# Optimization experiments

Measured on AMD Instinct MI355X. Metric: run time of the kernel, lower is better.

Reference implementation:

```python
import jax, jax.numpy as jnp
import numpy as np
from jax import lax

N_IN, N_H = 3, 2
N_REC = N_IN + N_H  # 5 qubits in the recurrent cell


def _ry(theta):
    # theta: (B,) -> (B, 2, 2) complex64 RY matrices
    c = jnp.cos(theta * 0.5).astype(jnp.complex64)
    s = jnp.sin(theta * 0.5).astype(jnp.complex64)
    return jnp.stack([jnp.stack([c, -s], -1), jnp.stack([s, c], -1)], -2)


def _rot(phi, theta, omega):
    # PennyLane Rot(phi, theta, omega) = RZ(omega) @ RY(theta) @ RZ(phi)
    c = jnp.cos(theta * 0.5)
    s = jnp.sin(theta * 0.5)
    ep = jnp.exp(-0.5j * (phi + omega))  # e^{-i(phi+omega)/2}
    em = jnp.exp(0.5j * (phi - omega))   # e^{+i(phi-omega)/2}
    m = jnp.stack([jnp.stack([ep * c, -em * s], -1),
                   jnp.stack([jnp.conj(em) * s, jnp.conj(ep) * c], -1)], -2)
    return m.astype(jnp.complex64)


def _apply1q(state, U, wire, n):
    # state: (B, 2**n); wire 0 is most significant (PennyLane convention)
    L, R = 2 ** wire, 2 ** (n - wire - 1)
    st = state.reshape(-1, L, 2, R)
    sub = 'bij,bljr->blir' if U.ndim == 3 else 'ij,bljr->blir'
    return jnp.einsum(sub, U, st).reshape(state.shape)


def _cnot_perm(c, t, n):
    # CNOT is a fixed basis permutation: flip target bit where control bit set
    cbit, tbit = 1 << (n - 1 - c), 1 << (n - 1 - t)
    idx = np.arange(2 ** n)
    return np.where(idx & cbit, idx ^ tbit, idx)


def _entangle(state, weights, n):
    # StronglyEntanglingLayers: per-wire Rot, then CNOT ring with range r
    n_layers = weights.shape[0]
    for l in range(n_layers):
        for w in range(n):
            state = _apply1q(state, _rot(weights[l, w, 0], weights[l, w, 1], weights[l, w, 2]), w, n)
        r = (l % (n - 1)) + 1
        for w in range(n):
            state = state[:, _cnot_perm(w, (w + r) % n, n)]
    return state


def _expz(state, wire, n):
    # <Z_wire> = P(0) - P(1)
    L, R = 2 ** wire, 2 ** (n - wire - 1)
    p = (state.real ** 2 + state.imag ** 2).reshape(-1, L, 2, R).sum((1, 3))
    return p[:, 0] - p[:, 1]


def _init_state(batch, n):
    s = jnp.zeros((batch, 2 ** n), jnp.complex64)
    return s.at[:, 0].set(1.0)


def _cell(x, h, w_rec):
    # batched qrnn_cell: RY-encode x on wires 0..2, h on wires 3..4, entangle, read Z(3),Z(4)
    state = _init_state(x.shape[0], N_REC)
    for i in range(N_IN):
        state = _apply1q(state, _ry(x[:, i]), i, N_REC)
    for j in range(N_H):
        state = _apply1q(state, _ry(h[:, j]), N_IN + j, N_REC)
    state = _entangle(state, w_rec, N_REC)
    return jnp.stack([_expz(state, N_IN + j, N_REC) for j in range(N_H)], -1)


def _readout(h, w_out):
    # batched qnn_readout: 2-qubit circuit, Z(0) expval
    state = _init_state(h.shape[0], N_H)
    for j in range(N_H):
        state = _apply1q(state, _ry(h[:, j]), j, N_H)
    state = _entangle(state, w_out, N_H)
    return _expz(state, 0, N_H)[:, None]


def setup_inputs() -> dict:
    key = jax.random.key(0)
    k1, k2, k3 = jax.random.split(key, 3)
    T, B = 32, 8192
    x_seq = jax.random.normal(k1, (T, B, N_IN), jnp.float32)
    w_rec = jax.random.normal(k2, (2, N_REC, 3), jnp.float32)
    w_out = jax.random.normal(k3, (2, N_H, 3), jnp.float32)
    return {"x_seq": x_seq, "w_rec": w_rec, "w_out": w_out}


def reference(x_seq, w_rec, w_out):
    B = x_seq.shape[1]

    def step(h, xt):
        return _cell(xt, h, w_rec), None

    h, _ = lax.scan(step, jnp.zeros((B, N_H), jnp.float32), x_seq)
    return _readout(h, w_out)  # (B, 1)
```

## Files before the change

### kernel.cpp

```cpp
#include <hip/hip_runtime.h>
#include <math.h>


constexpr int cnot_ct(int idx, int c, int t) {
    return (idx & (1 << (4 - c))) ? (idx ^ (1 << (4 - t))) : idx;
}
constexpr int Pfwd_ct(int x, int r) {
    for (int w = 4; w >= 0; --w) x = cnot_ct(x, w, (w + r) % 5);
    return x;
}
constexpr int Pinv_ct(int x, int r) {
    for (int w = 0; w <= 4; ++w) x = cnot_ct(x, w, (w + r) % 5);
    return x;
}
static_assert(Pinv_ct(Pfwd_ct(13, 1), 1) == 13, "inv1");
static_assert(Pinv_ct(Pfwd_ct(22, 2), 2) == 22, "inv2");

constexpr int GMASK[10] = {16, 8, 4, 2, 1,
                           Pfwd_ct(16,1), Pfwd_ct(8,1), Pfwd_ct(4,1), Pfwd_ct(2,1), Pfwd_ct(1,1)};
constexpr int fmask_l1(int pb) {
    int f = 0;
    for (int b = 0; b < 5; ++b) if ((Pinv_ct(1 << b, 1) >> pb) & 1) f |= 1 << b;
    return f;
}
constexpr int FMASK[10] = {16, 8, 4, 2, 1,
                           fmask_l1(4), fmask_l1(3), fmask_l1(2), fmask_l1(1), fmask_l1(0)};
constexpr int cinv_ct(int x) { return Pinv_ct(Pinv_ct(x, 1), 2); }
constexpr int fmask_fin(int pb) {
    int f = 0;
    for (int b = 0; b < 5; ++b) if ((cinv_ct(1 << b) >> pb) & 1) f |= 1 << b;
    return f;
}
constexpr int SF3 = fmask_fin(1);
constexpr int SF4 = fmask_fin(0);

constexpr bool gates_straddle() {
    for (int g = 0; g < 10; ++g)
        if (!(__builtin_popcount(GMASK[g] & FMASK[g]) & 1)) return false;
    return true;
}
static_assert(gates_straddle(), "GMASK/FMASK straddle");

constexpr unsigned span3_ct(int a, int b, int c) {
    unsigned m = 0;
    for (int i = 0; i < 8; ++i) {
        int v = ((i & 1) ? a : 0) ^ ((i & 2) ? b : 0) ^ ((i & 4) ? c : 0);
        m |= 1u << v;
    }
    return m;
}
static_assert(span3_ct(1, 2, 7) == 0xFFu, "butterfly {1,2,7} spans lanes 0..7");

__device__ __forceinline__ int pinv_rt(int x, int r) {
    #pragma unroll
    for (int w = 0; w < 5; ++w) {
        int cbit = 1 << (4 - w), tbit = 1 << (4 - ((w + r) % 5));
        if (x & cbit) x ^= tbit;
    }
    return x;
}

__device__ __forceinline__ float Wsel(int r, int d) {
    float b, c;
    if (d == 0)      { b =  2.f / 3.f; c = 0.f; }
    else if (d == 1) { b = -1.f / 3.f; c =  0.57735026918962576f; }
    else             { b = -1.f / 3.f; c = -0.57735026918962576f; }
    return (r == 0) ? (1.f / 3.f) : ((r == 1) ? b : c);
}

template<int CTRL> __device__ __forceinline__ float dppf(float x) {
    return __int_as_float(__builtin_amdgcn_mov_dpp(__float_as_int(x), CTRL, 0xF, 0xF, true));
}
template<int PL> __device__ __forceinline__ float mvf(float x) {
    if constexpr (PL == 1)      return dppf<0xB1>(x);
    else if constexpr (PL == 2) return dppf<0x4E>(x);
    else if constexpr (PL == 7) return dppf<0x141>(x);
    else if constexpr (PL == 8) return dppf<0x128>(x);
    else { static_assert(PL == 1 || PL == 2 || PL == 7 || PL == 8, "mask"); return x; }
}

template<int g>
__device__ __forceinline__ void gate_full(float (&ar)[32], float (&ai)[32],
                                          float c, float s) {
    constexpr int m = GMASK[g], F = FMASK[g];
    #pragma unroll
    for (int i = 0; i < 32; ++i) {
        if ((__builtin_popcount(i & F) & 1) == 0) {
            const int j = i ^ m;
            const float r0 = ar[i], i0 = ai[i], r1 = ar[j], i1 = ai[j];
            ar[i] = c * r0 - s * r1;  ai[i] = c * i0 - s * i1;
            ar[j] = s * r0 + c * r1;  ai[j] = s * i0 + c * i1;
        }
    }
}

__global__ __launch_bounds__(256, 2) void qrnn_fused(
    const float* __restrict__ x_seq, const float* __restrict__ w_rec,
    const float* __restrict__ w_out, float* __restrict__ out, int B) {

    __shared__ __align__(16) float4 xs4[16 * 33];
    __shared__ __align__(16) float A2s[18 * 28];
    __shared__ float CgS[10], SgS[10];
    __shared__ float P0c[32], P0s[32], E1c[32], E1s[32];
    __shared__ float RC[16];
    __shared__ __align__(16) float Cm_pool[16 * 19 * 33];
    float* const Qs  = Cm_pool;
    float* const P1s = Cm_pool + 512;

    const int tloc = threadIdx.x;
    const int grp  = tloc >> 4;
    const int k    = tloc & 15;
    const int b0   = blockIdx.x * 16;
    const int b    = b0 + grp;

    #pragma unroll
    for (int qq = 0; qq < 2; ++qq) {
        const int p = tloc + qq * 256;
        const int ts = p >> 4, lbs = p & 15;
        const int gidx = (ts * B + (b0 + lbs)) * 3;
        float4 v;
        v.x = x_seq[gidx]; v.y = x_seq[gidx + 1]; v.z = x_seq[gidx + 2]; v.w = 0.f;
        xs4[lbs * 33 + ts] = v;
    }

    if (tloc < 10) {
        const float th = w_rec[(tloc / 5) * 15 + (tloc % 5) * 3 + 1];
        CgS[tloc] = cosf(0.5f * th);
        SgS[tloc] = sinf(0.5f * th);
    } else if (tloc >= 32 && tloc < 96) {
        const int idx = tloc - 32;
        const int i = idx & 31;
        float ang = 0.f;
        if (idx < 32) {
            #pragma unroll
            for (int w = 0; w < 5; ++w)
                ang += (((i >> (4 - w)) & 1) ? 0.5f : -0.5f) * w_rec[w * 3 + 0];
            P0c[i] = cosf(ang); P0s[i] = sinf(ang);
        } else {
            const int j = pinv_rt(i, 1);
            #pragma unroll
            for (int w = 0; w < 5; ++w) {
                ang += (((i >> (4 - w)) & 1) ? 0.5f : -0.5f) * w_rec[w * 3 + 2];
                ang += (((j >> (4 - w)) & 1) ? 0.5f : -0.5f) * w_rec[15 + w * 3 + 0];
            }
            E1c[i] = cosf(ang); E1s[i] = sinf(ang);
        }
    } else if (tloc >= 96 && tloc < 100) {
        const int g = tloc - 96;
        const int li = g >> 1, w = g & 1;
        const float phi = w_out[li * 6 + w * 3 + 0];
        const float the = w_out[li * 6 + w * 3 + 1];
        const float ome = w_out[li * 6 + w * 3 + 2];
        const float cs = cosf(0.5f * the), ss = sinf(0.5f * the);
        const float cp = cosf(0.5f * (phi + ome)), sp = sinf(0.5f * (phi + ome));
        const float cm = cosf(0.5f * (phi - ome)), sm = sinf(0.5f * (phi - ome));
        RC[g * 4 + 0] = cp * cs;
        RC[g * 4 + 1] = -sp * cs;
        RC[g * 4 + 2] = cm * ss;
        RC[g * 4 + 3] = sm * ss;
    }
    __syncthreads();

    if (tloc < 243) {
        const int d0 = tloc / 81, d1 = (tloc / 27) % 3, d2 = (tloc / 9) % 3,
                  d3 = (tloc / 3) % 3, d4 = tloc % 3;
        constexpr float S3v = 0.86602540378443865f;
        const float f0c = (d0 == 0) ? 1.f : 0.5f;
        const float f0s = (d0 == 0) ? 0.f : ((d0 == 1) ? S3v : -S3v);
        const float f1c = (d1 == 0) ? 1.f : 0.5f;
        const float f1s = (d1 == 0) ? 0.f : ((d1 == 1) ? S3v : -S3v);
        const float f2c = (d2 == 0) ? 1.f : 0.5f;
        const float f2s = (d2 == 0) ? 0.f : ((d2 == 1) ? S3v : -S3v);
        const float f3c = (d3 == 0) ? 1.f : 0.5f;
        const float f3s = (d3 == 0) ? 0.f : ((d3 == 1) ? S3v : -S3v);
        const float f4c = (d4 == 0) ? 1.f : 0.5f;
        const float f4s = (d4 == 0) ? 0.f : ((d4 == 1) ? S3v : -S3v);

        float ar[32], ai[32];
        #pragma unroll
        for (int i = 0; i < 32; ++i) {
            const float bb = ((i & 16) ? f0s : f0c) * ((i & 8) ? f1s : f1c) *
                             ((i & 4) ? f2s : f2c) * ((i & 2) ? f3s : f3c) *
                             ((i & 1) ? f4s : f4c);
            ar[i] = bb * P0c[i]; ai[i] = bb * P0s[i];
        }
        gate_full<0>(ar, ai, CgS[0], SgS[0]);
        gate_full<1>(ar, ai, CgS[1], SgS[1]);
        gate_full<2>(ar, ai, CgS[2], SgS[2]);
        gate_full<3>(ar, ai, CgS[3], SgS[3]);
        gate_full<4>(ar, ai, CgS[4], SgS[4]);
        #pragma unroll
        for (int i = 0; i < 32; ++i) {
            const float nr = ar[i] * E1c[i] - ai[i] * E1s[i];
            const float ni = ar[i] * E1s[i] + ai[i] * E1c[i];
            ar[i] = nr; ai[i] = ni;
        }
        gate_full<5>(ar, ai, CgS[5], SgS[5]);
        gate_full<6>(ar, ai, CgS[6], SgS[6]);
        gate_full<7>(ar, ai, CgS[7], SgS[7]);
        gate_full<8>(ar, ai, CgS[8], SgS[8]);
        gate_full<9>(ar, ai, CgS[9], SgS[9]);
        float q0 = 0.f, q1 = 0.f;
        #pragma unroll
        for (int i = 0; i < 32; ++i) {
            const float p = ar[i] * ar[i] + ai[i] * ai[i];
            q0 += (__builtin_popcount(i & SF3) & 1) ? -p : p;
            q1 += (__builtin_popcount(i & SF4) & 1) ? -p : p;
        }
        *reinterpret_cast<float2*>(&Qs[tloc * 2]) = make_float2(q0, q1);
    }
    __syncthreads();

    for (int o = tloc; o < 486; o += 256) {
        const int j = o & 1, e = o >> 1;
        const int d012 = e / 9, pq = e % 9, pp = pq / 3, qq2 = pq % 3;
        float acc = 0.f;
        #pragma unroll
        for (int d3 = 0; d3 < 3; ++d3) {
            const float wp = Wsel(pp, d3);
            #pragma unroll
            for (int d4 = 0; d4 < 3; ++d4)
                acc = fmaf(wp * Wsel(qq2, d4), Qs[(d012 * 9 + d3 * 3 + d4) * 2 + j], acc);
        }
        P1s[(d012 * 9 + pq) * 2 + j] = acc;
    }
    __syncthreads();

    for (int o = tloc; o < 486; o += 256) {
        const int row = o / 27, col = o % 27;
        const int j = row / 9, pq = row % 9;
        const int a0 = col / 9, a1 = (col / 3) % 3, a2 = col % 3;
        float acc = 0.f;
        #pragma unroll
        for (int dd0 = 0; dd0 < 3; ++dd0) {
            const float w0 = Wsel(a0, dd0);
            #pragma unroll
            for (int dd1 = 0; dd1 < 3; ++dd1) {
                const float w01 = w0 * Wsel(a1, dd1);
                #pragma unroll
                for (int dd2 = 0; dd2 < 3; ++dd2)
                    acc = fmaf(w01 * Wsel(a2, dd2),
                               P1s[((dd0 * 9 + dd1 * 3 + dd2) * 9 + pq) * 2 + j], acc);
            }
        }
        A2s[row * 28 + col] = acc;
    }
    if (tloc < 18) A2s[tloc * 28 + 27] = 0.f;
    __syncthreads();

    constexpr float Kf = 0.15915494309189535f;
    float Xb0[28], Xb1[28];
    #pragma unroll
    for (int tt = 0; tt < 2; ++tt) {
        float* Xb = tt ? Xb1 : Xb0;
        const float4 xv = xs4[grp * 33 + k + 16 * tt];
        const float cx0 = __builtin_amdgcn_cosf(xv.x * Kf);
        const float sx0 = __builtin_amdgcn_cosf(fmaf(xv.x, Kf, -0.25f));
        const float cx1 = __builtin_amdgcn_cosf(xv.y * Kf);
        const float sx1 = __builtin_amdgcn_cosf(fmaf(xv.y, Kf, -0.25f));
        const float cx2 = __builtin_amdgcn_cosf(xv.z * Kf);
        const float sx2 = __builtin_amdgcn_cosf(fmaf(xv.z, Kf, -0.25f));
        Xb[0] = 1.f;  Xb[1] = cx2;       Xb[2] = sx2;
        Xb[3] = cx1;  Xb[4] = cx1 * cx2; Xb[5] = cx1 * sx2;
        Xb[6] = sx1;  Xb[7] = sx1 * cx2; Xb[8] = sx1 * sx2;
        #pragma unroll
        for (int i = 0; i < 9; ++i) { Xb[9 + i] = cx0 * Xb[i]; Xb[18 + i] = sx0 * Xb[i]; }
        Xb[27] = 0.f;
    }
    {
        const float4* Ap = (const float4*)A2s;
        float* const Cmg = Cm_pool + grp * (19 * 33);
        float4 bA[7], bB[7];
        #pragma unroll
        for (int i = 0; i < 7; ++i) bA[i] = Ap[i];
        #pragma unroll
        for (int i = 0; i < 7; ++i) bB[i] = Ap[7 + i];
        #pragma unroll 1
        for (int r = 0; r < 18; r += 2) {
            {
                float a00 = 0.f, a01 = 0.f, a10 = 0.f, a11 = 0.f;
                #pragma unroll
                for (int i = 0; i < 7; ++i) {
                    a00 = fmaf(bA[i].x, Xb0[4*i+0], a00); a00 = fmaf(bA[i].y, Xb0[4*i+1], a00);
                    a01 = fmaf(bA[i].z, Xb0[4*i+2], a01); a01 = fmaf(bA[i].w, Xb0[4*i+3], a01);
                    a10 = fmaf(bA[i].x, Xb1[4*i+0], a10); a10 = fmaf(bA[i].y, Xb1[4*i+1], a10);
                    a11 = fmaf(bA[i].z, Xb1[4*i+2], a11); a11 = fmaf(bA[i].w, Xb1[4*i+3], a11);
                }
                Cmg[r * 33 + k]      = a00 + a01;
                Cmg[r * 33 + k + 16] = a10 + a11;
                if (r < 16) {
                    #pragma unroll
                    for (int i = 0; i < 7; ++i) bA[i] = Ap[(r + 2) * 7 + i];
                }
            }
            {
                float a00 = 0.f, a01 = 0.f, a10 = 0.f, a11 = 0.f;
                #pragma unroll
                for (int i = 0; i < 7; ++i) {
                    a00 = fmaf(bB[i].x, Xb0[4*i+0], a00); a00 = fmaf(bB[i].y, Xb0[4*i+1], a00);
                    a01 = fmaf(bB[i].z, Xb0[4*i+2], a01); a01 = fmaf(bB[i].w, Xb0[4*i+3], a01);
                    a10 = fmaf(bB[i].x, Xb1[4*i+0], a10); a10 = fmaf(bB[i].y, Xb1[4*i+1], a10);
                    a11 = fmaf(bB[i].z, Xb1[4*i+2], a11); a11 = fmaf(bB[i].w, Xb1[4*i+3], a11);
                }
                Cmg[(r + 1) * 33 + k]      = a00 + a01;
                Cmg[(r + 1) * 33 + k + 16] = a10 + a11;
                if (r < 16) {
                    #pragma unroll
                    for (int i = 0; i < 7; ++i) bB[i] = Ap[(r + 3) * 7 + i];
                }
            }
        }
        Cmg[18 * 33 + k] = 0.f; Cmg[18 * 33 + k + 16] = 0.f;
    }

    const int jj = k >> 3;
    const int term = (k & 7) + 1;
    const int rowA = jj * 9 + term;
    const int rowB = (k == 0) ? 0 : ((k == 8) ? 9 : 18);
    const int p = term / 3, q = term % 3;
    const float* CA_ptr = Cm_pool + grp * (19 * 33) + rowA * 33;
    const float* CB_ptr = Cm_pool + grp * (19 * 33) + rowB * 33;

    float CAr[32], CBr[32];
    #pragma unroll
    for (int t = 0; t < 32; ++t) { CAr[t] = CA_ptr[t]; CBr[t] = CB_ptr[t]; }

    const float Kfu = (p == 0) ? 0.f : Kf;
    const float bu  = (p == 2) ? -0.25f : 0.f;
    const float Kfv = (q == 0) ? 0.f : Kf;
    const float bv  = (q == 2) ? -0.25f : 0.f;

    float h0 = 0.f, h1 = 0.f;
    #pragma unroll
    for (int t = 0; t < 32; ++t) {
        const float u = __builtin_amdgcn_cosf(fmaf(h0, Kfu, bu));
        const float v = __builtin_amdgcn_cosf(fmaf(h1, Kfv, bv));
        float val = fmaf(CAr[t], u * v, CBr[t]);
        val += mvf<1>(val);
        val += mvf<2>(val);
        val += mvf<7>(val);
        const float other = mvf<8>(val);
        h0 = (k & 8) ? other : val;
        h1 = (k & 8) ? val : other;
    }

    constexpr float K2 = 0.5f * 0.15915494309189535f;
    const float ch0 = __builtin_amdgcn_cosf(h0 * K2);
    const float sh0 = __builtin_amdgcn_cosf(fmaf(h0, K2, -0.25f));
    const float ch1 = __builtin_amdgcn_cosf(h1 * K2);
    const float sh1 = __builtin_amdgcn_cosf(fmaf(h1, K2, -0.25f));
    float vr0 = ch0 * ch1, vr1 = ch0 * sh1, vr2 = sh0 * ch1, vr3 = sh0 * sh1;
    float vi0 = 0.f, vi1 = 0.f, vi2 = 0.f, vi3 = 0.f;

    #pragma unroll
    for (int li = 0; li < 2; ++li) {
        #pragma unroll
        for (int w = 0; w < 2; ++w) {
            const int g = li * 2 + w;
            const float are = RC[g*4+0], aim = RC[g*4+1];
            const float bre = RC[g*4+2], bim = RC[g*4+3];
            #define AP2(r0, i0, r1, i1) do {                                  \
                float n0r = are*(r0) - aim*(i0) - bre*(r1) + bim*(i1);        \
                float n0i = are*(i0) + aim*(r0) - bre*(i1) - bim*(r1);        \
                float n1r = bre*(r0) + bim*(i0) + are*(r1) + aim*(i1);        \
                float n1i = bre*(i0) - bim*(r0) + are*(i1) - aim*(r1);        \
                r0 = n0r; i0 = n0i; r1 = n1r; i1 = n1i; } while (0)
            if (w == 0) { AP2(vr0, vi0, vr2, vi2); AP2(vr1, vi1, vr3, vi3); }
            else        { AP2(vr0, vi0, vr1, vi1); AP2(vr2, vi2, vr3, vi3); }
            #undef AP2
        }
        float tr1 = vr2, ti1 = vi2, tr2 = vr3, ti2 = vi3, tr3 = vr1, ti3 = vi1;
        vr1 = tr1; vi1 = ti1; vr2 = tr2; vi2 = ti2; vr3 = tr3; vi3 = ti3;
    }

    const float outv = (vr0 * vr0 + vi0 * vi0 + vr1 * vr1 + vi1 * vi1) -
                       (vr2 * vr2 + vi2 * vi2 + vr3 * vr3 + vi3 * vi3);
    if (k == 0) out[b] = outv;
}

extern "C" void kernel_launch(void* const* d_in, const int* in_sizes, int n_in,
                              void* d_out, int out_size, void* d_ws, size_t ws_size,
                              hipStream_t stream) {
    const float* x_seq = (const float*)d_in[0];
    const float* w_rec = (const float*)d_in[1];
    const float* w_out = (const float*)d_in[2];
    float* out = (float*)d_out;

    const int B = out_size;
    const int grid = (B * 16) / 256;

    hipLaunchKernelGGL(qrnn_fused, dim3(grid), dim3(256), 0, stream,
                       x_seq, w_rec, w_out, out, B);
}
```

Baseline: 73.68 us.

## Double batch rows per block and build first-layer state as a product state

Blocks now hold 32 batch elements with 512 threads instead of 16 with 256, so the per-block precompute of the transfer-matrix tables (243 circuit simulations and the two contraction passes) is shared by twice as many batch rows and runs in half as many blocks. The first-layer Rot gates are folded analytically into per-wire two-component vectors, and the 32-amplitude state is built by a tensor-product expansion instead of encoding followed by five butterfly gate passes. In exchange, shared memory per block roughly doubles, the larger block size may lower occupancy, and the unseen per-sequence code must agree with the new 32-row layout.

```diff
diff --git a/kernel.cpp b/kernel.cpp
--- a/kernel.cpp
+++ b/kernel.cpp
@@ -94,29 +94,30 @@
     }
 }
 
-__global__ __launch_bounds__(256, 2) void qrnn_fused(
+__global__ __launch_bounds__(512, 2) void qrnn_fused(
     const float* __restrict__ x_seq, const float* __restrict__ w_rec,
     const float* __restrict__ w_out, float* __restrict__ out, int B) {
 
-    __shared__ __align__(16) float4 xs4[16 * 33];
+    __shared__ __align__(16) float4 xs4[32 * 33];
     __shared__ __align__(16) float A2s[18 * 28];
     __shared__ float CgS[10], SgS[10];
-    __shared__ float P0c[32], P0s[32], E1c[32], E1s[32];
+    __shared__ float F0c[5], F0s[5];
+    __shared__ float E1c[32], E1s[32];
     __shared__ float RC[16];
-    __shared__ __align__(16) float Cm_pool[16 * 19 * 33];
+    __shared__ __align__(16) float Cm_pool[32 * 19 * 33];
     float* const Qs  = Cm_pool;
     float* const P1s = Cm_pool + 512;
 
     const int tloc = threadIdx.x;
     const int grp  = tloc >> 4;
     const int k    = tloc & 15;
-    const int b0   = blockIdx.x * 16;
+    const int b0   = blockIdx.x * 32;
     const int b    = b0 + grp;
 
     #pragma unroll
     for (int qq = 0; qq < 2; ++qq) {
-        const int p = tloc + qq * 256;
-        const int ts = p >> 4, lbs = p & 15;
+        const int p = tloc + qq * 512;
+        const int ts = p >> 5, lbs = p & 31;
         const int gidx = (ts * B + (b0 + lbs)) * 3;
         float4 v;
         v.x = x_seq[gidx]; v.y = x_seq[gidx + 1]; v.z = x_seq[gidx + 2]; v.w = 0.f;
@@ -127,24 +128,20 @@
         const float th = w_rec[(tloc / 5) * 15 + (tloc % 5) * 3 + 1];
         CgS[tloc] = cosf(0.5f * th);
         SgS[tloc] = sinf(0.5f * th);
-    } else if (tloc >= 32 && tloc < 96) {
-        const int idx = tloc - 32;
-        const int i = idx & 31;
+    } else if (tloc >= 16 && tloc < 21) {
+        const int w = tloc - 16;
+        const float ph = 0.5f * w_rec[w * 3 + 0];
+        F0c[w] = cosf(ph); F0s[w] = sinf(ph);
+    } else if (tloc >= 64 && tloc < 96) {
+        const int i = tloc - 64;
+        const int j = pinv_rt(i, 1);
         float ang = 0.f;
-        if (idx < 32) {
-            #pragma unroll
-            for (int w = 0; w < 5; ++w)
-                ang += (((i >> (4 - w)) & 1) ? 0.5f : -0.5f) * w_rec[w * 3 + 0];
-            P0c[i] = cosf(ang); P0s[i] = sinf(ang);
-        } else {
-            const int j = pinv_rt(i, 1);
-            #pragma unroll
-            for (int w = 0; w < 5; ++w) {
-                ang += (((i >> (4 - w)) & 1) ? 0.5f : -0.5f) * w_rec[w * 3 + 2];
-                ang += (((j >> (4 - w)) & 1) ? 0.5f : -0.5f) * w_rec[15 + w * 3 + 0];
-            }
-            E1c[i] = cosf(ang); E1s[i] = sinf(ang);
-        }
+        #pragma unroll
+        for (int w = 0; w < 5; ++w) {
+            ang += (((i >> (4 - w)) & 1) ? 0.5f : -0.5f) * w_rec[w * 3 + 2];
+            ang += (((j >> (4 - w)) & 1) ? 0.5f : -0.5f) * w_rec[15 + w * 3 + 0];
+        }
+        E1c[i] = cosf(ang); E1s[i] = sinf(ang);
     } else if (tloc >= 96 && tloc < 100) {
         const int g = tloc - 96;
         const int li = g >> 1, w = g & 1;
@@ -162,33 +159,37 @@
     __syncthreads();
 
     if (tloc < 243) {
-        const int d0 = tloc / 81, d1 = (tloc / 27) % 3, d2 = (tloc / 9) % 3,
-                  d3 = (tloc / 3) % 3, d4 = tloc % 3;
+        const int dsel[5] = {tloc / 81, (tloc / 27) % 3, (tloc / 9) % 3,
+                             (tloc / 3) % 3, tloc % 3};
         constexpr float S3v = 0.86602540378443865f;
-        const float f0c = (d0 == 0) ? 1.f : 0.5f;
-        const float f0s = (d0 == 0) ? 0.f : ((d0 == 1) ? S3v : -S3v);
-        const float f1c = (d1 == 0) ? 1.f : 0.5f;
-        const float f1s = (d1 == 0) ? 0.f : ((d1 == 1) ? S3v : -S3v);
-        const float f2c = (d2 == 0) ? 1.f : 0.5f;
-        const float f2s = (d2 == 0) ? 0.f : ((d2 == 1) ? S3v : -S3v);
-        const float f3c = (d3 == 0) ? 1.f : 0.5f;
-        const float f3s = (d3 == 0) ? 0.f : ((d3 == 1) ? S3v : -S3v);
-        const float f4c = (d4 == 0) ? 1.f : 0.5f;
-        const float f4s = (d4 == 0) ? 0.f : ((d4 == 1) ? S3v : -S3v);
-
+        float Arw[5], Aiw[5], Brw[5], Biw[5];
+        #pragma unroll
+        for (int w = 0; w < 5; ++w) {
+            const int d = dsel[w];
+            const float fc = (d == 0) ? 1.f : 0.5f;
+            const float fs = (d == 0) ? 0.f : ((d == 1) ? S3v : -S3v);
+            const float c = CgS[w], s = SgS[w];
+            const float t1 = fmaf(c, fc, -s * fs);
+            const float t2 = fmaf(c, fc,  s * fs);
+            const float t3 = fmaf(s, fc,  c * fs);
+            const float t4 = fmaf(c, fs, -s * fc);
+            Arw[w] =  F0c[w] * t1;  Aiw[w] = -F0s[w] * t2;
+            Brw[w] =  F0c[w] * t3;  Biw[w] =  F0s[w] * t4;
+        }
         float ar[32], ai[32];
-        #pragma unroll
-        for (int i = 0; i < 32; ++i) {
-            const float bb = ((i & 16) ? f0s : f0c) * ((i & 8) ? f1s : f1c) *
-                             ((i & 4) ? f2s : f2c) * ((i & 2) ? f3s : f3c) *
-                             ((i & 1) ? f4s : f4c);
-            ar[i] = bb * P0c[i]; ai[i] = bb * P0s[i];
-        }
-        gate_full<0>(ar, ai, CgS[0], SgS[0]);
-        gate_full<1>(ar, ai, CgS[1], SgS[1]);
-        gate_full<2>(ar, ai, CgS[2], SgS[2]);
-        gate_full<3>(ar, ai, CgS[3], SgS[3]);
-        gate_full<4>(ar, ai, CgS[4], SgS[4]);
+        ar[0] = Arw[0]; ai[0] = Aiw[0]; ar[1] = Brw[0]; ai[1] = Biw[0];
+        #pragma unroll
+        for (int w = 1; w < 5; ++w) {
+            const int n = 1 << w;
+            #pragma unroll
+            for (int m = n - 1; m >= 0; --m) {
+                const float orr = ar[m], oii = ai[m];
+                ar[2*m]   = fmaf(orr, Arw[w], -oii * Aiw[w]);
+                ai[2*m]   = fmaf(orr, Aiw[w],  oii * Arw[w]);
+                ar[2*m+1] = fmaf(orr, Brw[w], -oii * Biw[w]);
+                ai[2*m+1] = fmaf(orr, Biw[w],  oii * Brw[w]);
+            }
+        }
         #pragma unroll
         for (int i = 0; i < 32; ++i) {
             const float nr = ar[i] * E1c[i] - ai[i] * E1s[i];
@@ -211,7 +212,7 @@
     }
     __syncthreads();
 
-    for (int o = tloc; o < 486; o += 256) {
+    for (int o = tloc; o < 486; o += 512) {
         const int j = o & 1, e = o >> 1;
         const int d012 = e / 9, pq = e % 9, pp = pq / 3, qq2 = pq % 3;
         float acc = 0.f;
@@ -226,7 +227,7 @@
     }
     __syncthreads();
 
-    for (int o = tloc; o < 486; o += 256) {
+    for (int o = tloc; o < 486; o += 512) {
         const int row = o / 27, col = o % 27;
         const int j = row / 9, pq = row % 9;
         const int a0 = col / 9, a1 = (col / 3) % 3, a2 = col % 3;
@@ -387,8 +388,8 @@
     float* out = (float*)d_out;
 
     const int B = out_size;
-    const int grid = (B * 16) / 256;
-
-    hipLaunchKernelGGL(qrnn_fused, dim3(grid), dim3(256), 0, stream,
+    const int grid = B / 32;
+
+    hipLaunchKernelGGL(qrnn_fused, dim3(grid), dim3(512), 0, stream,
                        x_seq, w_rec, w_out, out, B);
 }
```

Measured after the change: 69.12 us. -6.2%, faster.
